# Kernel tuning notes

Measured on AMD Instinct MI355X. Metric: run time of the kernel, lower is better.

Reference implementation:

```python
import jax, jax.numpy as jnp
import numpy as np

B, S, D, H = 4, 1024, 1024, 16
DH = D // H  # 64
SCALE = 1.0 / np.sqrt(D)  # module uses 1/sqrt(d_model), not d_head


def _mh(t):
    # [B,S,D] -> [B*H,S,DH]
    b, s, _ = t.shape
    return t.reshape(b, s, H, DH).transpose(0, 2, 1, 3).reshape(b * H, s, DH)


def _shift(t):
    # pad one zero at FRONT of last dim, reinterpret (row-major) as [BH,L+1,S], drop first row
    bh, s, l = t.shape
    t = jnp.concatenate([jnp.zeros((bh, s, 1), t.dtype), t], axis=-1)
    return t.reshape(bh, l + 1, s)[:, 1:, :]


def setup_inputs() -> dict:
    key = jax.random.key(0)
    ks = jax.random.split(key, 12)
    w_sc = 1.0 / np.sqrt(D)
    return {
        "x": jax.random.normal(ks[0], (B, S, D), jnp.float32),
        "u": jax.random.normal(ks[1], (DH,), jnp.float32) * 0.02,
        "v": jax.random.normal(ks[2], (DH,), jnp.float32) * 0.02,
        "pos": jax.random.normal(ks[3], (B, S, D), jnp.float32),
        "Wq": jax.random.normal(ks[4], (D, D), jnp.float32) * w_sc,
        "bq": jnp.zeros((D,), jnp.float32),
        "Wk": jax.random.normal(ks[5], (D, D), jnp.float32) * w_sc,
        "bk": jnp.zeros((D,), jnp.float32),
        "Wv": jax.random.normal(ks[6], (D, D), jnp.float32) * w_sc,
        "bv": jnp.zeros((D,), jnp.float32),
        "Wc": jax.random.normal(ks[7], (D, D), jnp.float32) * w_sc,
        "bc": jnp.zeros((D,), jnp.float32),
    }


def reference(x, u, v, pos, Wq, bq, Wk, bk, Wv, bv, Wc, bc):
    q = _mh(x @ Wq.T + bq)      # [BH,S,DH]
    k = _mh(x @ Wk.T + bk)      # [BH,S,DH]
    w = _mh(x @ Wv.T + bv)      # [BH,S,DH]
    r = _mh(pos)                # [BH,S,DH]
    ac = jnp.einsum('bjk,bmk->bjm', q + u, k)          # content-content  [BH,S,S]
    bd = _shift(jnp.einsum('bjk,blk->bjl', q + v, r))  # content-position [BH,S,S]
    att = jax.nn.softmax((ac + bd) * SCALE, axis=-1)   # dropout is identity (eval)
    o = att @ w                                        # [BH,S,DH]
    o = o.reshape(B, H, S, DH).transpose(0, 2, 1, 3).reshape(B, S, D)
    return o @ Wc.T + bc
```

## Files before the change

### kernel.cpp

```cpp
#include <hip/hip_runtime.h>
#include <hip/hip_bf16.h>


typedef __bf16 bf16x8 __attribute__((ext_vector_type(8)));
typedef float  f32x4  __attribute__((ext_vector_type(4)));
typedef unsigned short u16x4 __attribute__((ext_vector_type(4)));

struct alignas(16) U128 { unsigned long long lo, hi; };

__device__ __forceinline__ bf16x8 ldg8(const __hip_bfloat16* p) {
    U128 u = *reinterpret_cast<const U128*>(p);
    return __builtin_bit_cast(bf16x8, u);
}

__device__ __forceinline__ __bf16 f2b(float f) {
    __hip_bfloat16 h = __float2bfloat16(f);
    return __builtin_bit_cast(__bf16, h);
}
__device__ __forceinline__ unsigned short f2bu(float f) {
    __hip_bfloat16 h = __float2bfloat16(f);
    return __builtin_bit_cast(unsigned short, h);
}
__device__ __forceinline__ float b2f(__bf16 b) {
    __hip_bfloat16 h = __builtin_bit_cast(__hip_bfloat16, b);
    return __bfloat162float(h);
}
__device__ __forceinline__ float bu2f(unsigned short u) {
    __hip_bfloat16 h = __builtin_bit_cast(__hip_bfloat16, u);
    return __bfloat162float(h);
}

__device__ __forceinline__ bf16x8 ldg8cvt(const float* p) {
    f32x4 a = *reinterpret_cast<const f32x4*>(p);
    f32x4 b = *reinterpret_cast<const f32x4*>(p + 4);
    bf16x8 r;
    r[0] = f2b(a[0]); r[1] = f2b(a[1]); r[2] = f2b(a[2]); r[3] = f2b(a[3]);
    r[4] = f2b(b[0]); r[5] = f2b(b[1]); r[6] = f2b(b[2]); r[7] = f2b(b[3]);
    return r;
}

#define MFMA16(a, b, c) __builtin_amdgcn_mfma_f32_16x16x32_bf16((a), (b), (c), 0, 0, 0)

__device__ __forceinline__ void gll16(const __hip_bfloat16* g, void* lds_wave_base) {
    __builtin_amdgcn_global_load_lds(
        (const __attribute__((address_space(1))) void*)g,
        (__attribute__((address_space(3))) void*)lds_wave_base,
        16, 0, 0);
}

__global__ __launch_bounds__(256) void cvt_kernel(
    const float* __restrict__ x,  const float* __restrict__ pos,
    const float* __restrict__ wq, const float* __restrict__ wk,
    const float* __restrict__ wv, const float* __restrict__ wc,
    __hip_bfloat16* __restrict__ xb, __hip_bfloat16* __restrict__ posb,
    __hip_bfloat16* __restrict__ wqkvb, __hip_bfloat16* __restrict__ wcb)
{
    const size_t base = ((size_t)blockIdx.x * 256 + threadIdx.x) * 8;
    const size_t M1 = (size_t)1 << 20;
    const float* src; __hip_bfloat16* dst; size_t o;
    if (base < 4*M1)        { src = x;   dst = xb;           o = base; }
    else if (base < 8*M1)   { src = pos; dst = posb;         o = base - 4*M1; }
    else if (base < 9*M1)   { src = wq;  dst = wqkvb;        o = base - 8*M1; }
    else if (base < 10*M1)  { src = wk;  dst = wqkvb + M1;   o = base - 9*M1; }
    else if (base < 11*M1)  { src = wv;  dst = wqkvb + 2*M1; o = base - 10*M1; }
    else                    { src = wc;  dst = wcb;          o = base - 11*M1; }
    *(bf16x8*)(dst + o) = ldg8cvt(src + o);
}

__global__ __launch_bounds__(256) void gemm_qkv(
    const __hip_bfloat16* __restrict__ A,
    const __hip_bfloat16* __restrict__ Bm,
    const float* __restrict__ bq, const float* __restrict__ bk,
    const float* __restrict__ bv, const float* __restrict__ u,
    __hip_bfloat16* __restrict__ Qu,
    __hip_bfloat16* __restrict__ Kb, __hip_bfloat16* __restrict__ Vt)
{
    __shared__ __hip_bfloat16 As[128 * 32];
    __shared__ __hip_bfloat16 Bs[128 * 32];

    const int tid  = threadIdx.x;
    const int lane = tid & 63, w = tid >> 6;
    const int quad = lane >> 4, c16 = lane & 15;
    const int wm = w >> 1, wn = w & 1;
    const int m0 = blockIdx.y * 128;
    const int n0 = blockIdx.x * 128;

    const int srow = w * 16 + (lane >> 2);
    const int scol = (lane & 3) * 8;
    const __hip_bfloat16* gA0 = A  + (size_t)(m0 + srow) * 1024 + scol;
    const __hip_bfloat16* gA1 = gA0 + (size_t)64 * 1024;
    const __hip_bfloat16* gB0 = Bm + (size_t)(n0 + srow) * 1024 + scol;
    const __hip_bfloat16* gB1 = gB0 + (size_t)64 * 1024;
    char* ldsA0 = (char*)As + (w << 10);
    char* ldsA1 = ldsA0 + 4096;
    char* ldsB0 = (char*)Bs + (w << 10);
    char* ldsB1 = ldsB0 + 4096;

    f32x4 acc[4][4] = {};

    for (int k0 = 0; k0 < 1024; k0 += 32) {
        gll16(gA0 + k0, ldsA0);
        gll16(gA1 + k0, ldsA1);
        gll16(gB0 + k0, ldsB0);
        gll16(gB1 + k0, ldsB1);
        __syncthreads();

        bf16x8 af[4], bfr[4];
        #pragma unroll
        for (int i = 0; i < 4; ++i) {
            af[i]  = *(const bf16x8*)&As[(wm * 64 + i * 16 + c16) * 32 + quad * 8];
            bfr[i] = *(const bf16x8*)&Bs[(wn * 64 + i * 16 + c16) * 32 + quad * 8];
        }
        #pragma unroll
        for (int mi = 0; mi < 4; ++mi)
            #pragma unroll
            for (int ni = 0; ni < 4; ++ni)
                acc[mi][ni] = MFMA16(af[mi], bfr[ni], acc[mi][ni]);
        __syncthreads();
    }

    #pragma unroll
    for (int mi = 0; mi < 4; ++mi) {
        #pragma unroll
        for (int ni = 0; ni < 4; ++ni) {
            const int m = m0 + wm * 64 + mi * 16 + quad * 4;
            const int n = n0 + wn * 64 + ni * 16 + c16;
            if (n < 1024) {
                const float b0 = bq[n] + u[n & 63];
                #pragma unroll
                for (int r = 0; r < 4; ++r)
                    Qu[(size_t)(m + r) * 1024 + n] =
                        __float2bfloat16(acc[mi][ni][r] + b0);
            } else if (n < 2048) {
                const int nn = n - 1024;
                const float b0 = bk[nn];
                #pragma unroll
                for (int r = 0; r < 4; ++r)
                    Kb[(size_t)(m + r) * 1024 + nn] =
                        __float2bfloat16(acc[mi][ni][r] + b0);
            } else {
                const int nn = n - 2048;
                const float b0 = bv[nn];
                const int d = nn & 63, hh = nn >> 6;
                const int bb = m >> 10, s = m & 1023;
                u16x4 pk;
                #pragma unroll
                for (int r = 0; r < 4; ++r)
                    pk[r] = f2bu(acc[mi][ni][r] + b0);
                *(u16x4*)&Vt[(((size_t)(bb * 16 + hh) * 64 + d) << 10) + s] = pk;
            }
        }
    }
}

__global__ __launch_bounds__(256) void gemm_fin(
    const __hip_bfloat16* __restrict__ A,
    const __hip_bfloat16* __restrict__ Bm,
    float* __restrict__ dout, const float* __restrict__ bc)
{
    __shared__ __hip_bfloat16 As[128 * 32];
    __shared__ __hip_bfloat16 Bs[128 * 32];

    const int tid  = threadIdx.x;
    const int lane = tid & 63, w = tid >> 6;
    const int quad = lane >> 4, c16 = lane & 15;
    const int wm = w >> 1, wn = w & 1;
    const int m0 = blockIdx.y * 128;
    const int n0 = blockIdx.x * 128;

    const int srow = w * 16 + (lane >> 2);
    const int scol = (lane & 3) * 8;
    const __hip_bfloat16* gA0 = A  + (size_t)(m0 + srow) * 1024 + scol;
    const __hip_bfloat16* gA1 = gA0 + (size_t)64 * 1024;
    const __hip_bfloat16* gB0 = Bm + (size_t)(n0 + srow) * 1024 + scol;
    const __hip_bfloat16* gB1 = gB0 + (size_t)64 * 1024;
    char* ldsA0 = (char*)As + (w << 10);
    char* ldsA1 = ldsA0 + 4096;
    char* ldsB0 = (char*)Bs + (w << 10);
    char* ldsB1 = ldsB0 + 4096;

    f32x4 acc[4][4] = {};

    for (int k0 = 0; k0 < 1024; k0 += 32) {
        gll16(gA0 + k0, ldsA0);
        gll16(gA1 + k0, ldsA1);
        gll16(gB0 + k0, ldsB0);
        gll16(gB1 + k0, ldsB1);
        __syncthreads();

        bf16x8 af[4], bfr[4];
        #pragma unroll
        for (int i = 0; i < 4; ++i) {
            af[i]  = *(const bf16x8*)&As[(wm * 64 + i * 16 + c16) * 32 + quad * 8];
            bfr[i] = *(const bf16x8*)&Bs[(wn * 64 + i * 16 + c16) * 32 + quad * 8];
        }
        #pragma unroll
        for (int mi = 0; mi < 4; ++mi)
            #pragma unroll
            for (int ni = 0; ni < 4; ++ni)
                acc[mi][ni] = MFMA16(af[mi], bfr[ni], acc[mi][ni]);
        __syncthreads();
    }

    #pragma unroll
    for (int mi = 0; mi < 4; ++mi) {
        #pragma unroll
        for (int ni = 0; ni < 4; ++ni) {
            const int m = m0 + wm * 64 + mi * 16 + quad * 4;
            const int n = n0 + wn * 64 + ni * 16 + c16;
            const float b0 = bc[n];
            #pragma unroll
            for (int r = 0; r < 4; ++r)
                dout[(size_t)(m + r) * 1024 + n] = acc[mi][ni][r] + b0;
        }
    }
}

__device__ __forceinline__ int lidx16(int row, int c) {
    return (row << 10) + ((((c >> 3) ^ row) << 3) | (c & 7));
}

__global__ __launch_bounds__(512, 2) void attn_kernel(
    const __hip_bfloat16* __restrict__ Qu,
    const __hip_bfloat16* __restrict__ Kb,
    const __hip_bfloat16* __restrict__ Posb,
    const __hip_bfloat16* __restrict__ Vt,
    const float* __restrict__ uvec, const float* __restrict__ vvec,
    __hip_bfloat16* __restrict__ O)
{
    __shared__ __attribute__((aligned(16))) __hip_bfloat16 Ls[64 * 1024];
    __shared__ float Wsum[64 * 8];
    __shared__ float rs[64];

    const int tid  = threadIdx.x;
    const int lane = tid & 63, w = tid >> 6;
    const int quad = lane >> 4, c16 = lane & 15;
    const int i0 = blockIdx.y * 64;
    const int bh = blockIdx.x;
    const int b = bh >> 4, h = bh & 15;
    const size_t headoff = (size_t)h * 64;
    const size_t tokbase = (size_t)b * 1024;
    const int j2 = i0 + 64;
    const bool havej2 = (j2 < 1024);

    if (tid < 64) {
        const int i = i0 + tid;
        if (i + 1 < 1024) Ls[lidx16(tid, i + 1)] = __float2bfloat16(0.f);
    }

    const __hip_bfloat16* qup0 =
        Qu + (tokbase + i0 + c16) * 1024 + headoff + quad * 8;

    {
        bf16x8 a[4][2];
        #pragma unroll
        for (int g = 0; g < 4; ++g) {
            a[g][0] = ldg8(qup0 + (size_t)g * 16 * 1024);
            a[g][1] = ldg8(qup0 + (size_t)g * 16 * 1024 + 32);
            #pragma unroll
            for (int j = 0; j < 8; ++j) {
                const int d = quad * 8 + j;
                a[g][0][j] = f2b(b2f(a[g][0][j]) + (vvec[d] - uvec[d]));
                a[g][1][j] = f2b(b2f(a[g][1][j]) + (vvec[d + 32] - uvec[d + 32]));
            }
        }
        bf16x8 a4[2];
        if (havej2) {
            a4[0] = ldg8(qup0 + (size_t)64 * 1024);
            a4[1] = ldg8(qup0 + (size_t)64 * 1024 + 32);
            #pragma unroll
            for (int j = 0; j < 8; ++j) {
                const int d = quad * 8 + j;
                a4[0][j] = f2b(b2f(a4[0][j]) + (vvec[d] - uvec[d]));
                a4[1][j] = f2b(b2f(a4[1][j]) + (vvec[d + 32] - uvec[d + 32]));
            }
        }
        for (int t = 0; t < 8; ++t) {
            const int l0 = w * 128 + t * 16;
            const __hip_bfloat16* rp =
                Posb + (tokbase + l0 + c16) * 1024 + headoff + quad * 8;
            const bf16x8 r0 = ldg8(rp);
            const bf16x8 r1 = ldg8(rp + 32);
            const int lq = l0 + quad * 4;
            #pragma unroll
            for (int g = 0; g < 4; ++g) {
                f32x4 c = (f32x4){0.f, 0.f, 0.f, 0.f};
                c = MFMA16(r0, a[g][0], c);
                c = MFMA16(r1, a[g][1], c);
                const int jl = g * 16 + c16;
                const int base2 = lq + i0 + jl + 1;
                const int rwm1 = jl - 1;
                #pragma unroll
                for (int r = 0; r < 4; ++r) {
                    const int t1 = base2 + r;
                    const int cc = t1 & 1023;
                    const int rw = rwm1 + (t1 >> 10);
                    if (rw >= 0)
                        Ls[lidx16(rw, cc)] = __float2bfloat16(c[r]);
                }
            }
            if (havej2) {
                f32x4 c = (f32x4){0.f, 0.f, 0.f, 0.f};
                c = MFMA16(r0, a4[0], c);
                c = MFMA16(r1, a4[1], c);
                if (c16 == 0) {
                    #pragma unroll
                    for (int r = 0; r < 4; ++r) {
                        const int cc = lq + r + i0 + 65;
                        if (cc < 1024)
                            Ls[lidx16(63, cc)] = __float2bfloat16(c[r]);
                    }
                }
            }
        }
    }
    __syncthreads();

    {
        bf16x8 au[4][2];
        #pragma unroll
        for (int g = 0; g < 4; ++g) {
            au[g][0] = ldg8(qup0 + (size_t)g * 16 * 1024);
            au[g][1] = ldg8(qup0 + (size_t)g * 16 * 1024 + 32);
        }
        const float C1 = 1.44269504f * 0.03125f;
        const float C2 = -5.77078016f;
        float rsum[4] = {0.f, 0.f, 0.f, 0.f};
        for (int t = 0; t < 8; ++t) {
            const int c0 = w * 128 + t * 16;
            const __hip_bfloat16* kp =
                Kb + (tokbase + c0 + c16) * 1024 + headoff + quad * 8;
            const bf16x8 k0 = ldg8(kp);
            const bf16x8 k1 = ldg8(kp + 32);
            const int cc0 = c0 + quad * 4;
            #pragma unroll
            for (int g = 0; g < 4; ++g) {
                f32x4 c = (f32x4){0.f, 0.f, 0.f, 0.f};
                c = MFMA16(k0, au[g][0], c);
                c = MFMA16(k1, au[g][1], c);
                const int jl = g * 16 + c16;
                const int idx = lidx16(jl, cc0);
                const u16x4 bd = *(const u16x4*)&Ls[idx];
                u16x4 pk;
                float s4 = 0.f;
                #pragma unroll
                for (int r = 0; r < 4; ++r) {
                    const float lg = bu2f(bd[r]) + c[r];
                    const float p = __builtin_amdgcn_exp2f(fmaf(lg, C1, C2));
                    s4 += p;
                    pk[r] = f2bu(p);
                }
                *(u16x4*)&Ls[idx] = pk;
                s4 += __shfl_xor(s4, 16);
                s4 += __shfl_xor(s4, 32);
                rsum[g] += s4;
            }
        }
        if (lane < 16) {
            #pragma unroll
            for (int g = 0; g < 4; ++g)
                Wsum[(g * 16 + lane) * 8 + w] = rsum[g];
        }
    }
    __syncthreads();

    if (tid < 64) {
        float s = 0.f;
        #pragma unroll
        for (int k = 0; k < 8; ++k) s += Wsum[tid * 8 + k];
        rs[tid] = 1.f / s;
    }
    __syncthreads();

    {
        const int d0 = (w & 3) * 16;
        const int kh = w >> 2;
        const __hip_bfloat16* vp =
            Vt + ((size_t)bh * 64 + d0 + c16) * 1024 + quad * 8;
        f32x4 acc[4] = {};
        for (int kk = kh * 512; kk < kh * 512 + 512; kk += 32) {
            const bf16x8 vld = ldg8(vp + kk);
            #pragma unroll
            for (int g = 0; g < 4; ++g) {
                const bf16x8 p =
                    *(const bf16x8*)&Ls[lidx16(g * 16 + c16, kk + quad * 8)];
                acc[g] = MFMA16(p, vld, acc[g]);
            }
        }
        __syncthreads();
        float* Lf = (float*)Ls;
        const int sbase = (w & 3) * 1024;
        if (kh == 1) {
            #pragma unroll
            for (int g = 0; g < 4; ++g)
                #pragma unroll
                for (int r = 0; r < 4; ++r)
                    Lf[sbase + g * 256 + (quad * 4 + r) * 16 + c16] = acc[g][r];
        }
        __syncthreads();
        if (kh == 0) {
            #pragma unroll
            for (int g = 0; g < 4; ++g)
                #pragma unroll
                for (int r = 0; r < 4; ++r) {
                    const int il = g * 16 + quad * 4 + r;
                    const float val =
                        (acc[g][r] + Lf[sbase + g * 256 + (quad * 4 + r) * 16 + c16])
                        * rs[il];
                    const int i = i0 + il;
                    const int d = d0 + c16;
                    O[(tokbase + i) * 1024 + headoff + d] = __float2bfloat16(val);
                }
        }
    }
}

extern "C" void kernel_launch(void* const* d_in, const int* in_sizes, int n_in,
                              void* d_out, int out_size, void* d_ws, size_t ws_size,
                              hipStream_t stream)
{
    const float* x   = (const float*)d_in[0];
    const float* u   = (const float*)d_in[1];
    const float* v   = (const float*)d_in[2];
    const float* pos = (const float*)d_in[3];
    const float* Wq  = (const float*)d_in[4];
    const float* bq  = (const float*)d_in[5];
    const float* Wk  = (const float*)d_in[6];
    const float* bk  = (const float*)d_in[7];
    const float* Wv  = (const float*)d_in[8];
    const float* bv  = (const float*)d_in[9];
    const float* Wc  = (const float*)d_in[10];
    const float* bc  = (const float*)d_in[11];

    const size_t MB = (size_t)1 << 20;
    char* ws = (char*)d_ws;
    __hip_bfloat16* Qu    = (__hip_bfloat16*)(ws + 0 * MB);
    __hip_bfloat16* Kb    = (__hip_bfloat16*)(ws + 8 * MB);
    __hip_bfloat16* Vt    = (__hip_bfloat16*)(ws + 16 * MB);
    __hip_bfloat16* xb    = (__hip_bfloat16*)(ws + 24 * MB);
    __hip_bfloat16* O     = (__hip_bfloat16*)(ws + 24 * MB);
    __hip_bfloat16* Posb  = (__hip_bfloat16*)(ws + 32 * MB);
    __hip_bfloat16* Wqkvb = (__hip_bfloat16*)(ws + 40 * MB);
    __hip_bfloat16* Wcb   = (__hip_bfloat16*)(ws + 46 * MB);

    cvt_kernel<<<6144, 256, 0, stream>>>(x, pos, Wq, Wk, Wv, Wc,
                                         xb, Posb, Wqkvb, Wcb);

    gemm_qkv<<<dim3(24, 32), dim3(256), 0, stream>>>(
        xb, Wqkvb, bq, bk, bv, u, Qu, Kb, Vt);

    attn_kernel<<<dim3(64, 16), dim3(512), 0, stream>>>(
        Qu, Kb, Posb, Vt, u, v, O);

    gemm_fin<<<dim3(8, 32), dim3(256), 0, stream>>>(
        O, Wcb, (float*)d_out, bc);
}
```

Before: 266.6 us.

## Fold softmax scale into Q, hoist q+v setup, defer row-sum shuffles, shrink final GEMM tiles

Multiplies Qu by the combined log2e/sqrt(D) factor in the QKV GEMM epilogue, so the attention softmax computes exp2 directly with no per-element FMA. The constant max-subtraction offset is dropped, which is only safe while logits stay small. The Q fragments are loaded once and reused for both the position and content passes, with v-u precomputed. The cross-lane row-sum shuffles move out of the inner loop to the end. The output-projection GEMM switches from 128x128 to 64x64 tiles to launch more blocks, at the cost of less reuse per block.

```diff
diff --git a/kernel.cpp b/kernel.cpp
--- a/kernel.cpp
+++ b/kernel.cpp
@@ -40,6 +40,8 @@
 }
 
 #define MFMA16(a, b, c) __builtin_amdgcn_mfma_f32_16x16x32_bf16((a), (b), (c), 0, 0, 0)
+
+#define C1F 0.0450843334f
 
 __device__ __forceinline__ void gll16(const __hip_bfloat16* g, void* lds_wave_base) {
     __builtin_amdgcn_global_load_lds(
@@ -130,7 +132,7 @@
                 #pragma unroll
                 for (int r = 0; r < 4; ++r)
                     Qu[(size_t)(m + r) * 1024 + n] =
-                        __float2bfloat16(acc[mi][ni][r] + b0);
+                        __float2bfloat16((acc[mi][ni][r] + b0) * C1F);
             } else if (n < 2048) {
                 const int nn = n - 1024;
                 const float b0 = bk[nn];
@@ -153,61 +155,55 @@
     }
 }
 
-__global__ __launch_bounds__(256) void gemm_fin(
+__global__ __launch_bounds__(256) void gemm_fin64(
     const __hip_bfloat16* __restrict__ A,
     const __hip_bfloat16* __restrict__ Bm,
     float* __restrict__ dout, const float* __restrict__ bc)
 {
-    __shared__ __hip_bfloat16 As[128 * 32];
-    __shared__ __hip_bfloat16 Bs[128 * 32];
+    __shared__ __hip_bfloat16 As[64 * 32];
+    __shared__ __hip_bfloat16 Bs[64 * 32];
 
     const int tid  = threadIdx.x;
     const int lane = tid & 63, w = tid >> 6;
     const int quad = lane >> 4, c16 = lane & 15;
     const int wm = w >> 1, wn = w & 1;
-    const int m0 = blockIdx.y * 128;
-    const int n0 = blockIdx.x * 128;
+    const int m0 = blockIdx.y * 64;
+    const int n0 = blockIdx.x * 64;
 
     const int srow = w * 16 + (lane >> 2);
     const int scol = (lane & 3) * 8;
-    const __hip_bfloat16* gA0 = A  + (size_t)(m0 + srow) * 1024 + scol;
-    const __hip_bfloat16* gA1 = gA0 + (size_t)64 * 1024;
-    const __hip_bfloat16* gB0 = Bm + (size_t)(n0 + srow) * 1024 + scol;
-    const __hip_bfloat16* gB1 = gB0 + (size_t)64 * 1024;
-    char* ldsA0 = (char*)As + (w << 10);
-    char* ldsA1 = ldsA0 + 4096;
-    char* ldsB0 = (char*)Bs + (w << 10);
-    char* ldsB1 = ldsB0 + 4096;
-
-    f32x4 acc[4][4] = {};
+    const __hip_bfloat16* gA = A  + (size_t)(m0 + srow) * 1024 + scol;
+    const __hip_bfloat16* gB = Bm + (size_t)(n0 + srow) * 1024 + scol;
+    char* ldsA = (char*)As + (w << 10);
+    char* ldsB = (char*)Bs + (w << 10);
+
+    f32x4 acc[2][2] = {};
 
     for (int k0 = 0; k0 < 1024; k0 += 32) {
-        gll16(gA0 + k0, ldsA0);
-        gll16(gA1 + k0, ldsA1);
-        gll16(gB0 + k0, ldsB0);
-        gll16(gB1 + k0, ldsB1);
-        __syncthreads();
-
-        bf16x8 af[4], bfr[4];
-        #pragma unroll
-        for (int i = 0; i < 4; ++i) {
-            af[i]  = *(const bf16x8*)&As[(wm * 64 + i * 16 + c16) * 32 + quad * 8];
-            bfr[i] = *(const bf16x8*)&Bs[(wn * 64 + i * 16 + c16) * 32 + quad * 8];
-        }
-        #pragma unroll
-        for (int mi = 0; mi < 4; ++mi)
-            #pragma unroll
-            for (int ni = 0; ni < 4; ++ni)
+        gll16(gA + k0, ldsA);
+        gll16(gB + k0, ldsB);
+        __syncthreads();
+
+        bf16x8 af[2], bfr[2];
+        #pragma unroll
+        for (int i = 0; i < 2; ++i) {
+            af[i]  = *(const bf16x8*)&As[(wm * 32 + i * 16 + c16) * 32 + quad * 8];
+            bfr[i] = *(const bf16x8*)&Bs[(wn * 32 + i * 16 + c16) * 32 + quad * 8];
+        }
+        #pragma unroll
+        for (int mi = 0; mi < 2; ++mi)
+            #pragma unroll
+            for (int ni = 0; ni < 2; ++ni)
                 acc[mi][ni] = MFMA16(af[mi], bfr[ni], acc[mi][ni]);
         __syncthreads();
     }
 
     #pragma unroll
-    for (int mi = 0; mi < 4; ++mi) {
-        #pragma unroll
-        for (int ni = 0; ni < 4; ++ni) {
-            const int m = m0 + wm * 64 + mi * 16 + quad * 4;
-            const int n = n0 + wn * 64 + ni * 16 + c16;
+    for (int mi = 0; mi < 2; ++mi) {
+        #pragma unroll
+        for (int ni = 0; ni < 2; ++ni) {
+            const int m = m0 + wm * 32 + mi * 16 + quad * 4;
+            const int n = n0 + wn * 32 + ni * 16 + c16;
             const float b0 = bc[n];
             #pragma unroll
             for (int r = 0; r < 4; ++r)
@@ -251,28 +247,34 @@
     const __hip_bfloat16* qup0 =
         Qu + (tokbase + i0 + c16) * 1024 + headoff + quad * 8;
 
+    float dvuA[8], dvuB[8];
+    #pragma unroll
+    for (int j = 0; j < 8; ++j) {
+        const int d = quad * 8 + j;
+        dvuA[j] = (vvec[d]      - uvec[d])      * C1F;
+        dvuB[j] = (vvec[d + 32] - uvec[d + 32]) * C1F;
+    }
+    bf16x8 au[4][2], av[4][2];
+    #pragma unroll
+    for (int g = 0; g < 4; ++g) {
+        au[g][0] = ldg8(qup0 + (size_t)g * 16 * 1024);
+        au[g][1] = ldg8(qup0 + (size_t)g * 16 * 1024 + 32);
+        #pragma unroll
+        for (int j = 0; j < 8; ++j) {
+            av[g][0][j] = f2b(b2f(au[g][0][j]) + dvuA[j]);
+            av[g][1][j] = f2b(b2f(au[g][1][j]) + dvuB[j]);
+        }
+    }
+
     {
-        bf16x8 a[4][2];
-        #pragma unroll
-        for (int g = 0; g < 4; ++g) {
-            a[g][0] = ldg8(qup0 + (size_t)g * 16 * 1024);
-            a[g][1] = ldg8(qup0 + (size_t)g * 16 * 1024 + 32);
-            #pragma unroll
-            for (int j = 0; j < 8; ++j) {
-                const int d = quad * 8 + j;
-                a[g][0][j] = f2b(b2f(a[g][0][j]) + (vvec[d] - uvec[d]));
-                a[g][1][j] = f2b(b2f(a[g][1][j]) + (vvec[d + 32] - uvec[d + 32]));
-            }
-        }
         bf16x8 a4[2];
         if (havej2) {
             a4[0] = ldg8(qup0 + (size_t)64 * 1024);
             a4[1] = ldg8(qup0 + (size_t)64 * 1024 + 32);
             #pragma unroll
             for (int j = 0; j < 8; ++j) {
-                const int d = quad * 8 + j;
-                a4[0][j] = f2b(b2f(a4[0][j]) + (vvec[d] - uvec[d]));
-                a4[1][j] = f2b(b2f(a4[1][j]) + (vvec[d + 32] - uvec[d + 32]));
+                a4[0][j] = f2b(b2f(a4[0][j]) + dvuA[j]);
+                a4[1][j] = f2b(b2f(a4[1][j]) + dvuB[j]);
             }
         }
         for (int t = 0; t < 8; ++t) {
@@ -285,8 +287,8 @@
             #pragma unroll
             for (int g = 0; g < 4; ++g) {
                 f32x4 c = (f32x4){0.f, 0.f, 0.f, 0.f};
-                c = MFMA16(r0, a[g][0], c);
-                c = MFMA16(r1, a[g][1], c);
+                c = MFMA16(r0, av[g][0], c);
+                c = MFMA16(r1, av[g][1], c);
                 const int jl = g * 16 + c16;
                 const int base2 = lq + i0 + jl + 1;
                 const int rwm1 = jl - 1;
@@ -317,14 +319,6 @@
     __syncthreads();
 
     {
-        bf16x8 au[4][2];
-        #pragma unroll
-        for (int g = 0; g < 4; ++g) {
-            au[g][0] = ldg8(qup0 + (size_t)g * 16 * 1024);
-            au[g][1] = ldg8(qup0 + (size_t)g * 16 * 1024 + 32);
-        }
-        const float C1 = 1.44269504f * 0.03125f;
-        const float C2 = -5.77078016f;
         float rsum[4] = {0.f, 0.f, 0.f, 0.f};
         for (int t = 0; t < 8; ++t) {
             const int c0 = w * 128 + t * 16;
@@ -345,21 +339,21 @@
                 float s4 = 0.f;
                 #pragma unroll
                 for (int r = 0; r < 4; ++r) {
-                    const float lg = bu2f(bd[r]) + c[r];
-                    const float p = __builtin_amdgcn_exp2f(fmaf(lg, C1, C2));
+                    const float p =
+                        __builtin_amdgcn_exp2f(bu2f(bd[r]) + c[r]);
                     s4 += p;
                     pk[r] = f2bu(p);
                 }
                 *(u16x4*)&Ls[idx] = pk;
-                s4 += __shfl_xor(s4, 16);
-                s4 += __shfl_xor(s4, 32);
                 rsum[g] += s4;
             }
         }
-        if (lane < 16) {
-            #pragma unroll
-            for (int g = 0; g < 4; ++g)
-                Wsum[(g * 16 + lane) * 8 + w] = rsum[g];
+        #pragma unroll
+        for (int g = 0; g < 4; ++g) {
+            float s = rsum[g];
+            s += __shfl_xor(s, 16);
+            s += __shfl_xor(s, 32);
+            if (lane < 16) Wsum[(g * 16 + lane) * 8 + w] = s;
         }
     }
     __syncthreads();
@@ -452,6 +446,6 @@
     attn_kernel<<<dim3(64, 16), dim3(512), 0, stream>>>(
         Qu, Kb, Posb, Vt, u, v, O);
 
-    gemm_fin<<<dim3(8, 32), dim3(256), 0, stream>>>(
+    gemm_fin64<<<dim3(16, 64), dim3(256), 0, stream>>>(
         O, Wcb, (float*)d_out, bc);
 }
```

New measurement: 255.7 us. 1.04x faster.
